# Performance work log

Measured on AMD Instinct MI355X. Metric: run time of the kernel, lower is better.

Reference implementation:

```python
import jax, jax.numpy as jnp
import numpy as np

N_NODES = 50000   # hypergraph nodes
N_EDGES = 20000   # hyperedges
M = 400000        # node-edge incidences (node copies)
L = 800000        # inner GIN graph edges per side
HID = 128
IN_DIM = 128
B = 32            # graphs in batch
C = 10            # num_classes
N_LAYERS = 2
INNER = 2         # inner_num_layers
BN_EPS = 1e-5


def setup_inputs() -> dict:
    key = jax.random.key(0)
    ks = jax.random.split(key, 16)
    s = 0.05
    inp = {}
    inp["x_N"] = jax.random.normal(ks[0], (N_NODES, IN_DIM), jnp.float32)
    # embedding linear
    inp["We"] = jax.random.normal(ks[1], (IN_DIM, HID), jnp.float32) * s
    inp["be"] = jnp.zeros((HID,), jnp.float32)
    # GIN params: [outer_layer, direction(N2E/E2N), inner_conv, mlp_linear, hid, hid]
    inp["Wg"] = jax.random.normal(ks[2], (N_LAYERS, 2, INNER, 2, HID, HID), jnp.float32) * s
    inp["bg"] = jnp.zeros((N_LAYERS, 2, INNER, 2, HID), jnp.float32)
    inp["eps_g"] = jnp.zeros((N_LAYERS, 2, INNER), jnp.float32)
    # eval-mode BatchNorm affine params per inner conv
    inp["gamma"] = jnp.ones((N_LAYERS, 2, INNER, HID), jnp.float32)
    inp["beta"] = jnp.zeros((N_LAYERS, 2, INNER, HID), jnp.float32)
    # per-layer prediction heads
    inp["Wp"] = jax.random.normal(ks[3], (N_LAYERS + 1, HID, C), jnp.float32) * s
    inp["bp"] = jnp.zeros((N_LAYERS + 1, C), jnp.float32)
    # index tensors
    inp["ori_node_idx"] = jax.random.randint(ks[4], (M,), 0, N_NODES)
    inp["node2edge"] = jax.random.randint(ks[5], (M,), 0, N_EDGES)
    inp["edge_index_N"] = jax.random.randint(ks[6], (2, L), 0, M)
    inp["ori_edge_idx"] = jax.random.randint(ks[7], (M,), 0, N_EDGES)
    inp["edge2node"] = jax.random.randint(ks[8], (M,), 0, N_NODES)
    inp["edge_index_E"] = jax.random.randint(ks[9], (2, L), 0, M)
    inp["batch"] = jax.random.randint(ks[10], (M,), 0, B)
    return inp


def _gin(x, src, dst, Wg, bg, eps, gamma, beta):
    # GIN over the copy graph: h = MLP((1+eps)*x + sum_{j->i} x_j), BN (eval), ReLU between convs
    inv_std = 1.0 / jnp.sqrt(1.0 + BN_EPS)
    n = x.shape[0]
    for l in range(INNER):
        agg = jax.ops.segment_sum(x[src], dst, num_segments=n)
        h = (1.0 + eps[l]) * x + agg
        h = jax.nn.relu(h @ Wg[l, 0] + bg[l, 0])
        h = h @ Wg[l, 1] + bg[l, 1]
        h = gamma[l] * h * inv_std + beta[l]
        x = jax.nn.relu(h) if l < INNER - 1 else h
    return x


def reference(x_N, We, be, Wg, bg, eps_g, gamma, beta, Wp, bp,
              ori_node_idx, node2edge, edge_index_N,
              ori_edge_idx, edge2node, edge_index_E, batch):
    node_x = x_N @ We + be                       # [N, HID]
    xs = [node_x]
    for i in range(N_LAYERS):
        # node -> edge: gather copies, inner GIN, segment-sum pool over hyperedges
        nx = node_x[ori_node_idx]                # [M, HID]
        nx = _gin(nx, edge_index_N[0], edge_index_N[1],
                  Wg[i, 0], bg[i, 0], eps_g[i, 0], gamma[i, 0], beta[i, 0])
        edge_x = jax.ops.segment_sum(nx, node2edge, num_segments=N_EDGES)
        edge_x = jax.nn.relu(edge_x)             # EdgeUpdate (dropout off in eval)
        # edge -> node
        ex = edge_x[ori_edge_idx]                # [M, HID]
        ex = _gin(ex, edge_index_E[0], edge_index_E[1],
                  Wg[i, 1], bg[i, 1], eps_g[i, 1], gamma[i, 1], beta[i, 1])
        node_x = jax.ops.segment_sum(ex, edge2node, num_segments=N_NODES)
        node_x = jax.nn.relu(node_x)             # NodeUpdate
        xs.append(node_x)
    score = jnp.zeros((B, C), x_N.dtype)
    for i, x in enumerate(xs):
        pooled = jax.ops.segment_sum(x[ori_node_idx], batch, num_segments=B)
        score = score + pooled @ Wp[i] + bp[i]
    return score
```

## Files before the change

### kernel.cpp

```cpp
#include <hip/hip_runtime.h>
#include <hip/hip_bf16.h>

#define HID 128
static const int N_NODES = 50000;
static const int N_EDGES = 20000;
static const int M_COPIES = 400000;
static const int L_EDGES = 800000;
static const int NBATCH = 32;
static const int NCLS = 10;
#define INV_STD 0.9999950000374997f
#define IDX_CAP 384

typedef __attribute__((ext_vector_type(4))) float f32x4;
typedef __attribute__((ext_vector_type(8))) short short8;
typedef __attribute__((ext_vector_type(8))) unsigned short ushort8;
typedef __attribute__((ext_vector_type(4))) unsigned short u16x4;

__device__ __forceinline__ float bf2f(unsigned short u) {
    union { unsigned u; float f; } v; v.u = ((unsigned)u) << 16; return v.f;
}
__device__ __forceinline__ unsigned short f2bf(float f) {
    union { float f; unsigned u; } v; v.f = f;
    unsigned r = v.u + 0x7FFFu + ((v.u >> 16) & 1u);
    return (unsigned short)(r >> 16);
}
__device__ __forceinline__ void gatomic_add(float* p, float v) {
    unsafeAtomicAdd(p, v);
}

template<int H>
__device__ __forceinline__ void mfma_eighth(const unsigned short* Ws, const short8* xv,
                                            f32x4* acc, int quad, int ln) {
#pragma unroll
    for (int kc = 0; kc < 4; ++kc) {
        short8 wa = *(const short8*)(Ws + (((kc * 4 + quad) * 16) + ln) * 8);
        acc[H] = __builtin_amdgcn_mfma_f32_16x16x32_bf16(wa, xv[kc], acc[H], 0, 0, 0);
    }
}

__global__ __launch_bounds__(256) void prep_w(const float* __restrict__ We,
                                              const float* __restrict__ Wg,
                                              unsigned short* __restrict__ Wt) {
    int t = blockIdx.x * 256 + threadIdx.x;
    if (t >= 17 * 16384) return;
    int mat = t >> 14, rem = t & 16383;
    int n = rem >> 7, k = rem & 127;
    const float* src = (mat == 0) ? We : (Wg + (size_t)(mat - 1) * 16384);
    Wt[t] = f2bf(src[k * 128 + n]);
}

__global__ __launch_bounds__(256) void hist_k(const int* __restrict__ idx, int n,
                                              int* __restrict__ cnt) {
    int t = blockIdx.x * 256 + threadIdx.x;
    if (t < n) atomicAdd(&cnt[idx[t]], 1);
}

__global__ __launch_bounds__(256) void scan1_k(int* __restrict__ a, int n,
                                               int* __restrict__ part) {
    __shared__ int s[256];
    int i = blockIdx.x * 256 + threadIdx.x;
    int v = (i < n) ? a[i] : 0;
    s[threadIdx.x] = v;
    __syncthreads();
#pragma unroll
    for (int d = 1; d < 256; d <<= 1) {
        int t = (threadIdx.x >= d) ? s[threadIdx.x - d] : 0;
        __syncthreads();
        s[threadIdx.x] += t;
        __syncthreads();
    }
    if (i < n) a[i] = s[threadIdx.x] - v;
    if (threadIdx.x == 255) part[blockIdx.x] = s[255];
}

__global__ __launch_bounds__(256) void scan2_k(int* __restrict__ part, int nb) {
    __shared__ int s[256];
    __shared__ int carry;
    if (threadIdx.x == 0) carry = 0;
    __syncthreads();
    for (int base = 0; base < nb; base += 256) {
        int i = base + threadIdx.x;
        int v = (i < nb) ? part[i] : 0;
        s[threadIdx.x] = v;
        __syncthreads();
#pragma unroll
        for (int d = 1; d < 256; d <<= 1) {
            int t = (threadIdx.x >= d) ? s[threadIdx.x - d] : 0;
            __syncthreads();
            s[threadIdx.x] += t;
            __syncthreads();
        }
        if (i < nb) part[i] = carry + s[threadIdx.x] - v;
        __syncthreads();
        if (threadIdx.x == 0) carry += s[255];
        __syncthreads();
    }
}

__global__ __launch_bounds__(256) void scan3_k(int* __restrict__ a, int n,
                                               const int* __restrict__ part) {
    int i = blockIdx.x * 256 + threadIdx.x;
    if (i < n) a[i] += part[blockIdx.x];
}

__global__ __launch_bounds__(256) void fill_edge_k(
    const int* __restrict__ src, const int* __restrict__ dst,
    const int* __restrict__ remap, int n, int* __restrict__ off,
    int* __restrict__ srcs, int* __restrict__ comps) {
    int e = blockIdx.x * 256 + threadIdx.x;
    if (e >= n) return;
    int d = dst[e];
    int pos = atomicAdd(&off[d], 1);
    int s = src[e];
    srcs[pos] = s;
    comps[pos] = remap[s];
}

__global__ __launch_bounds__(256) void fill_pool_k(
    const int* __restrict__ seg, int n, int* __restrict__ off,
    int* __restrict__ items) {
    int m = blockIdx.x * 256 + threadIdx.x;
    if (m >= n) return;
    int pos = atomicAdd(&off[seg[m]], 1);
    items[pos] = m;
}

__global__ __launch_bounds__(256) void segsum_pool(
    const unsigned short* __restrict__ tbl, const int* __restrict__ off,
    const int* __restrict__ items, unsigned short* __restrict__ out, int nseg)
{
    int wave = threadIdx.x >> 6, lane = threadIdx.x & 63;
    int seg = blockIdx.x * 4 + wave;
    if (seg >= nseg) return;
    int start = (seg == 0) ? 0 : off[seg - 1];
    int end = off[seg];
    int g = lane & 15, sub = lane >> 4;
    float a[8] = {0.f, 0.f, 0.f, 0.f, 0.f, 0.f, 0.f, 0.f};
    for (int p = start + sub; p < end; p += 4) {
        int r = items[p];
        ushort8 v = *(const ushort8*)(tbl + (size_t)r * 128 + g * 8);
#pragma unroll
        for (int j = 0; j < 8; ++j) a[j] += bf2f(v[j]);
    }
#pragma unroll
    for (int j = 0; j < 8; ++j) {
        a[j] += __shfl_xor(a[j], 16, 64);
        a[j] += __shfl_xor(a[j], 32, 64);
    }
    if (sub == 0) {
        ushort8 ov;
#pragma unroll
        for (int j = 0; j < 8; ++j) ov[j] = f2bf(fmaxf(a[j], 0.f));
        *(ushort8*)(out + (size_t)seg * 128 + g * 8) = ov;
    }
}

template<bool CONV0>
__global__ __launch_bounds__(256, 7) void fused_conv(
    const unsigned short* __restrict__ tbl,
    const int* __restrict__ self_idx,
    const int* __restrict__ off, const int* __restrict__ items,
    const float* __restrict__ eps_ptr,
    const unsigned short* __restrict__ W1t, const float* __restrict__ b1,
    const unsigned short* __restrict__ W2t, const float* __restrict__ b2,
    const float* __restrict__ gam, const float* __restrict__ bet,
    unsigned short* __restrict__ out)
{
    __shared__ __align__(16) unsigned short Xs[16 * 64 * 8];
    __shared__ __align__(16) unsigned short Ws[16 * 16 * 8];
    __shared__ int sIdx[IDX_CAP];
    __shared__ int meta[192];
    const int tid = threadIdx.x;
    const int row0 = blockIdx.x * 64;

    const int bstart = (row0 == 0) ? 0 : off[row0 - 1];
    const int cnt = off[row0 + 63] - bstart;
    const bool useLds = (cnt <= IDX_CAP);

    if (tid < 64) {
        int gr = row0 + tid;
        meta[tid]       = (gr == 0) ? 0 : off[gr - 1];
        meta[64 + tid]  = off[gr];
        meta[128 + tid] = CONV0 ? self_idx[gr] : gr;
    }
    {
        int n = tid >> 4, gg = tid & 15;
        *(short8*)(Ws + (gg * 16 + n) * 8) = *(const short8*)(W1t + n * 128 + gg * 8);
    }
    if (useLds)
        for (int i = tid; i < cnt; i += 256) sIdx[i] = items[bstart + i];
    __syncthreads();

    const float e = 1.0f + eps_ptr[0];
    const int g = tid & 15;
    const int rb = tid >> 4;
#pragma unroll
    for (int i = 0; i < 4; ++i) {
        int r = rb + 16 * i;
        int start = meta[r], end = meta[64 + r], self = meta[128 + r];
        float a[8];
        ushort8 u = *(const ushort8*)(tbl + (size_t)self * 128 + g * 8);
#pragma unroll
        for (int j = 0; j < 8; ++j) a[j] = e * bf2f(u[j]);
        if (useLds) {
            int pos = start - bstart, pe = end - bstart;
            for (; pos + 2 <= pe; pos += 2) {
                int i0 = sIdx[pos], i1 = sIdx[pos + 1];
                ushort8 v0 = *(const ushort8*)(tbl + (size_t)i0 * 128 + g * 8);
                ushort8 v1 = *(const ushort8*)(tbl + (size_t)i1 * 128 + g * 8);
#pragma unroll
                for (int j = 0; j < 8; ++j) a[j] += bf2f(v0[j]) + bf2f(v1[j]);
            }
            if (pos < pe) {
                int i0 = sIdx[pos];
                ushort8 v0 = *(const ushort8*)(tbl + (size_t)i0 * 128 + g * 8);
#pragma unroll
                for (int j = 0; j < 8; ++j) a[j] += bf2f(v0[j]);
            }
        } else {
            for (int pos = start; pos < end; ++pos) {
                int rr = items[pos];
                ushort8 v = *(const ushort8*)(tbl + (size_t)rr * 128 + g * 8);
#pragma unroll
                for (int j = 0; j < 8; ++j) a[j] += bf2f(v[j]);
            }
        }
        ushort8 xv;
#pragma unroll
        for (int j = 0; j < 8; ++j) xv[j] = f2bf(a[j]);
        *(ushort8*)(Xs + (g * 64 + r) * 8) = xv;
    }
    __syncthreads();

    const int lane = tid & 63;
    const int ln = lane & 15, quad = lane >> 4;
    const int row = (tid >> 6) * 16 + ln;

    short8 xb[4];
#pragma unroll
    for (int kc = 0; kc < 4; ++kc)
        xb[kc] = *(const short8*)(Xs + ((kc * 4 + quad) * 64 + row) * 8);

    f32x4 acc[8];
#pragma unroll
    for (int t = 0; t < 8; ++t) acc[t] = (f32x4){0.f, 0.f, 0.f, 0.f};

    mfma_eighth<0>(Ws, xb, acc, quad, ln);
#pragma unroll
    for (int h = 1; h < 8; ++h) {
        __syncthreads();
        {
            int n = tid >> 4, gg = tid & 15;
            *(short8*)(Ws + (gg * 16 + n) * 8) = *(const short8*)(W1t + (h * 16 + n) * 128 + gg * 8);
        }
        __syncthreads();
        switch (h) {
            case 1: mfma_eighth<1>(Ws, xb, acc, quad, ln); break;
            case 2: mfma_eighth<2>(Ws, xb, acc, quad, ln); break;
            case 3: mfma_eighth<3>(Ws, xb, acc, quad, ln); break;
            case 4: mfma_eighth<4>(Ws, xb, acc, quad, ln); break;
            case 5: mfma_eighth<5>(Ws, xb, acc, quad, ln); break;
            case 6: mfma_eighth<6>(Ws, xb, acc, quad, ln); break;
            default: mfma_eighth<7>(Ws, xb, acc, quad, ln); break;
        }
    }
    {
        const int j0 = (quad & 1) * 4;
#pragma unroll
        for (int t = 0; t < 8; ++t) {
            int p0 = t * 16 + quad * 4;
            f32x4 bv = *(const f32x4*)(b1 + p0);
            u16x4 hp;
#pragma unroll
            for (int i = 0; i < 4; ++i) hp[i] = f2bf(fmaxf(acc[t][i] + bv[i], 0.f));
            *(u16x4*)(Xs + ((p0 >> 3) * 64 + row) * 8 + j0) = hp;
        }
    }
    __syncthreads();
    {
        int n = tid >> 4, gg = tid & 15;
        *(short8*)(Ws + (gg * 16 + n) * 8) = *(const short8*)(W2t + n * 128 + gg * 8);
    }
    __syncthreads();

    short8 hb[4];
#pragma unroll
    for (int kc = 0; kc < 4; ++kc)
        hb[kc] = *(const short8*)(Xs + ((kc * 4 + quad) * 64 + row) * 8);

#pragma unroll
    for (int t = 0; t < 8; ++t) acc[t] = (f32x4){0.f, 0.f, 0.f, 0.f};

    mfma_eighth<0>(Ws, hb, acc, quad, ln);
#pragma unroll
    for (int h = 1; h < 8; ++h) {
        __syncthreads();
        {
            int n = tid >> 4, gg = tid & 15;
            *(short8*)(Ws + (gg * 16 + n) * 8) = *(const short8*)(W2t + (h * 16 + n) * 128 + gg * 8);
        }
        __syncthreads();
        switch (h) {
            case 1: mfma_eighth<1>(Ws, hb, acc, quad, ln); break;
            case 2: mfma_eighth<2>(Ws, hb, acc, quad, ln); break;
            case 3: mfma_eighth<3>(Ws, hb, acc, quad, ln); break;
            case 4: mfma_eighth<4>(Ws, hb, acc, quad, ln); break;
            case 5: mfma_eighth<5>(Ws, hb, acc, quad, ln); break;
            case 6: mfma_eighth<6>(Ws, hb, acc, quad, ln); break;
            default: mfma_eighth<7>(Ws, hb, acc, quad, ln); break;
        }
    }

    const int m = row0 + row;
#pragma unroll
    for (int t = 0; t < 8; ++t) {
        int n0 = t * 16 + quad * 4;
        f32x4 bv = *(const f32x4*)(b2 + n0);
        f32x4 gv = *(const f32x4*)(gam + n0);
        f32x4 tv = *(const f32x4*)(bet + n0);
        u16x4 op;
#pragma unroll
        for (int i = 0; i < 4; ++i) {
            float h = acc[t][i] + bv[i];
            h = gv[i] * h * INV_STD + tv[i];
            if (CONV0) h = fmaxf(h, 0.f);
            op[i] = f2bf(h);
        }
        *(u16x4*)(out + (size_t)m * 128 + n0) = op;
    }
}

__global__ __launch_bounds__(256) void gemm_embed(
    const float* __restrict__ in, const unsigned short* __restrict__ Wt,
    const float* __restrict__ bias, unsigned short* __restrict__ out_bf, int rows)
{
    __shared__ __align__(16) unsigned short Xs[16 * 64 * 8];
    __shared__ __align__(16) unsigned short Ws[16 * 128 * 8];
    int tid = threadIdx.x;
    int row0 = blockIdx.x * 64;
#pragma unroll
    for (int i = 0; i < 8; ++i) {
        int chunk = tid + i * 256;
        int n = chunk >> 4, g = chunk & 15;
        *(short8*)(Ws + (g * 128 + n) * 8) = *(const short8*)(Wt + n * 128 + g * 8);
    }
#pragma unroll
    for (int i = 0; i < 4; ++i) {
        int chunk = tid + i * 256;
        int r = chunk >> 4, g = chunk & 15;
        int gr = row0 + r;
        ushort8 v;
        if (gr < rows) {
            const float* p = in + (size_t)gr * 128 + g * 8;
            f32x4 a0 = *(const f32x4*)p;
            f32x4 a1 = *(const f32x4*)(p + 4);
#pragma unroll
            for (int j = 0; j < 4; ++j) { v[j] = f2bf(a0[j]); v[4 + j] = f2bf(a1[j]); }
        } else {
#pragma unroll
            for (int j = 0; j < 8; ++j) v[j] = 0;
        }
        *(ushort8*)(Xs + (g * 64 + r) * 8) = v;
    }
    __syncthreads();
    int wave = tid >> 6, lane = tid & 63;
    int m0 = wave * 16;
    int ln = lane & 15, quad = lane >> 4;
    f32x4 acc[8];
#pragma unroll
    for (int t = 0; t < 8; ++t) acc[t] = (f32x4){0.f, 0.f, 0.f, 0.f};
#pragma unroll
    for (int kc = 0; kc < 4; ++kc) {
        int g = kc * 4 + quad;
        short8 a = *(const short8*)(Xs + (g * 64 + m0 + ln) * 8);
#pragma unroll
        for (int t = 0; t < 8; ++t) {
            short8 b = *(const short8*)(Ws + (g * 128 + t * 16 + ln) * 8);
            acc[t] = __builtin_amdgcn_mfma_f32_16x16x32_bf16(a, b, acc[t], 0, 0, 0);
        }
    }
#pragma unroll
    for (int t = 0; t < 8; ++t) {
        int col = t * 16 + ln;
        float bi = bias[col];
#pragma unroll
        for (int i = 0; i < 4; ++i) {
            int gr = row0 + m0 + quad * 4 + i;
            if (gr < rows) out_bf[(size_t)gr * 128 + col] = f2bf(acc[t][i] + bi);
        }
    }
}

template<bool ACCUM>
__global__ __launch_bounds__(256) void proj_y(
    const unsigned short* __restrict__ nx, const float* __restrict__ Wp,
    float* __restrict__ y, int rows)
{
    __shared__ float Wl[HID * NCLS];
    for (int i = threadIdx.x; i < HID * NCLS; i += 256) Wl[i] = Wp[i];
    __syncthreads();
    int r = blockIdx.x * 256 + threadIdx.x;
    if (r >= rows) return;
    float acc[NCLS];
#pragma unroll
    for (int c = 0; c < NCLS; ++c) acc[c] = 0.f;
    const unsigned short* xp = nx + (size_t)r * 128;
#pragma unroll 4
    for (int g = 0; g < 16; ++g) {
        ushort8 u = *(const ushort8*)(xp + g * 8);
#pragma unroll
        for (int j = 0; j < 8; ++j) {
            float xv = bf2f(u[j]);
            const float* w = Wl + (g * 8 + j) * NCLS;
#pragma unroll
            for (int c = 0; c < NCLS; ++c) acc[c] += xv * w[c];
        }
    }
    float* yp = y + (size_t)r * NCLS;
#pragma unroll
    for (int c = 0; c < NCLS; ++c) {
        if (ACCUM) yp[c] += acc[c];
        else yp[c] = acc[c];
    }
}

__global__ __launch_bounds__(256) void score_scatter(
    const float* __restrict__ y, const int* __restrict__ ori,
    const int* __restrict__ batch, float* __restrict__ score)
{
    __shared__ float sc[NBATCH * NCLS];
    for (int i = threadIdx.x; i < NBATCH * NCLS; i += 256) sc[i] = 0.f;
    __syncthreads();
    int stride = gridDim.x * 256;
    for (int m = blockIdx.x * 256 + threadIdx.x; m < M_COPIES; m += stride) {
        int r = ori[m], b = batch[m];
        const float* yp = y + (size_t)r * NCLS;
#pragma unroll
        for (int c = 0; c < NCLS; ++c)
            __hip_atomic_fetch_add(&sc[b * NCLS + c], yp[c],
                                   __ATOMIC_RELAXED, __HIP_MEMORY_SCOPE_WORKGROUP);
    }
    __syncthreads();
    for (int i = threadIdx.x; i < NBATCH * NCLS; i += 256) gatomic_add(score + i, sc[i]);
}

__global__ void score_final(const float* __restrict__ score, const float* __restrict__ bp,
                            float* __restrict__ out)
{
    int t = threadIdx.x;
    if (t >= NBATCH * NCLS) return;
    int c = t % NCLS;
    out[t] = score[t] + bp[c] + bp[NCLS + c] + bp[2 * NCLS + c];
}

__global__ void fill_sentinel(float* out, int n, float enc) {
    int t = blockIdx.x * 64 + threadIdx.x;
    if (t < n) out[t] = enc;
}

static inline void build_csr_edge(const int* src, const int* dst, const int* remap,
                                  int nitem, int nseg, int* off, int* part,
                                  int* srcs, int* comps, hipStream_t stream) {
    int nb = (nseg + 255) / 256;
    (void)hipMemsetAsync(off, 0, (size_t)nseg * 4, stream);
    hist_k<<<(nitem + 255) / 256, 256, 0, stream>>>(dst, nitem, off);
    scan1_k<<<nb, 256, 0, stream>>>(off, nseg, part);
    scan2_k<<<1, 256, 0, stream>>>(part, nb);
    scan3_k<<<nb, 256, 0, stream>>>(off, nseg, part);
    fill_edge_k<<<(nitem + 255) / 256, 256, 0, stream>>>(src, dst, remap, nitem, off, srcs, comps);
}
static inline void build_csr_pool(const int* seg, int nitem, int nseg,
                                  int* off, int* part, int* items, hipStream_t stream) {
    int nb = (nseg + 255) / 256;
    (void)hipMemsetAsync(off, 0, (size_t)nseg * 4, stream);
    hist_k<<<(nitem + 255) / 256, 256, 0, stream>>>(seg, nitem, off);
    scan1_k<<<nb, 256, 0, stream>>>(off, nseg, part);
    scan2_k<<<1, 256, 0, stream>>>(part, nb);
    scan3_k<<<nb, 256, 0, stream>>>(off, nseg, part);
    fill_pool_k<<<(nitem + 255) / 256, 256, 0, stream>>>(seg, nitem, off, items);
}

extern "C" void kernel_launch(void* const* d_in, const int* in_sizes, int n_in,
                              void* d_out, int out_size, void* d_ws, size_t ws_size,
                              hipStream_t stream) {
    const float* x_N    = (const float*)d_in[0];
    const float* We     = (const float*)d_in[1];
    const float* be     = (const float*)d_in[2];
    const float* Wg     = (const float*)d_in[3];
    const float* bg     = (const float*)d_in[4];
    const float* eps_g  = (const float*)d_in[5];
    const float* gam    = (const float*)d_in[6];
    const float* bet    = (const float*)d_in[7];
    const float* Wp     = (const float*)d_in[8];
    const float* bp     = (const float*)d_in[9];
    const int* ori_node = (const int*)d_in[10];
    const int* node2edge= (const int*)d_in[11];
    const int* eiN      = (const int*)d_in[12];
    const int* ori_edge = (const int*)d_in[13];
    const int* edge2node= (const int*)d_in[14];
    const int* eiE      = (const int*)d_in[15];
    const int* batch    = (const int*)d_in[16];

    char* p = (char*)d_ws;
    auto take = [&](size_t n) { char* r = p; p += (n + 255) & ~(size_t)255; return r; };
    unsigned short* Wt  = (unsigned short*)take((size_t)17 * 16384 * 2);
    unsigned short* Xb  = (unsigned short*)take((size_t)M_COPIES * 128 * 2);
    unsigned short* Xb2 = (unsigned short*)take((size_t)M_COPIES * 128 * 2);
    unsigned short* nx  = (unsigned short*)take((size_t)N_NODES * 128 * 2);
    unsigned short* ex  = (unsigned short*)take((size_t)N_EDGES * 128 * 2);
    float* y            = (float*)take((size_t)N_NODES * NCLS * 4);
    float* score        = (float*)take((size_t)NBATCH * NCLS * 4);
    int* offN           = (int*)take((size_t)M_COPIES * 4);
    int* offE           = (int*)take((size_t)M_COPIES * 4);
    int* off_n2e        = (int*)take((size_t)N_EDGES * 4);
    int* off_e2n        = (int*)take((size_t)N_NODES * 4);
    int* srcsN          = (int*)take((size_t)L_EDGES * 4);
    int* compsN         = (int*)take((size_t)L_EDGES * 4);
    int* srcsE          = (int*)take((size_t)L_EDGES * 4);
    int* compsE         = (int*)take((size_t)L_EDGES * 4);
    int* it_n2e         = (int*)take((size_t)M_COPIES * 4);
    int* it_e2n         = (int*)take((size_t)M_COPIES * 4);
    int* part           = (int*)take((size_t)2048 * 4);
    size_t need = (size_t)(p - (char*)d_ws);
    if (need > ws_size) {
        fill_sentinel<<<(out_size + 63) / 64, 64, 0, stream>>>(
            (float*)d_out, out_size, 1.0e9f + (float)ws_size);
        return;
    }

    prep_w<<<1088, 256, 0, stream>>>(We, Wg, Wt);
    (void)hipMemsetAsync(score, 0, (size_t)NBATCH * NCLS * 4, stream);

    build_csr_edge(eiN, eiN + L_EDGES, ori_node, L_EDGES, M_COPIES, offN, part, srcsN, compsN, stream);
    build_csr_edge(eiE, eiE + L_EDGES, ori_edge, L_EDGES, M_COPIES, offE, part, srcsE, compsE, stream);
    build_csr_pool(node2edge, M_COPIES, N_EDGES, off_n2e, part, it_n2e, stream);
    build_csr_pool(edge2node, M_COPIES, N_NODES, off_e2n, part, it_e2n, stream);

    gemm_embed<<<(N_NODES + 63) / 64, 256, 0, stream>>>(x_N, Wt, be, nx, N_NODES);
    proj_y<false><<<(N_NODES + 255) / 256, 256, 0, stream>>>(nx, Wp, y, N_NODES);

    const int MBLK = M_COPIES / 64;
    for (int layer = 0; layer < 2; ++layer) {
        for (int dir = 0; dir < 2; ++dir) {
            int cj0 = layer * 4 + dir * 2;
            int cj1 = cj0 + 1;
            const unsigned short* base = (dir == 0) ? nx : ex;
            const int* selfI = (dir == 0) ? ori_node : ori_edge;
            const int* offD  = (dir == 0) ? offN : offE;
            const int* srcsD = (dir == 0) ? srcsN : srcsE;
            const int* compD = (dir == 0) ? compsN : compsE;

            fused_conv<true><<<MBLK, 256, 0, stream>>>(
                base, selfI, offD, compD, eps_g + cj0,
                Wt + (size_t)(1 + cj0 * 2) * 16384, bg + (cj0 * 2) * 128,
                Wt + (size_t)(1 + cj0 * 2 + 1) * 16384, bg + (cj0 * 2 + 1) * 128,
                gam + cj0 * 128, bet + cj0 * 128, Xb);
            fused_conv<false><<<MBLK, 256, 0, stream>>>(
                Xb, nullptr, offD, srcsD, eps_g + cj1,
                Wt + (size_t)(1 + cj1 * 2) * 16384, bg + (cj1 * 2) * 128,
                Wt + (size_t)(1 + cj1 * 2 + 1) * 16384, bg + (cj1 * 2 + 1) * 128,
                gam + cj1 * 128, bet + cj1 * 128, Xb2);
            if (dir == 0) {
                segsum_pool<<<(N_EDGES + 3) / 4, 256, 0, stream>>>(
                    Xb2, off_n2e, it_n2e, ex, N_EDGES);
            } else {
                segsum_pool<<<(N_NODES + 3) / 4, 256, 0, stream>>>(
                    Xb2, off_e2n, it_e2n, nx, N_NODES);
                proj_y<true><<<(N_NODES + 255) / 256, 256, 0, stream>>>(
                    nx, Wp + (layer + 1) * HID * NCLS, y, N_NODES);
            }
        }
    }
    score_scatter<<<256, 256, 0, stream>>>(y, ori_node, batch, score);
    score_final<<<1, 320, 0, stream>>>(score, bp, (float*)d_out);
}
```

Before: 1.529 ms.

## Read GEMM weights directly from global memory and swizzle the activation LDS tile

New measurement: 2.485 ms. 62.6% more time.

```diff
diff --git a/kernel.cpp b/kernel.cpp
--- a/kernel.cpp
+++ b/kernel.cpp
@@ -28,14 +28,9 @@
     unsafeAtomicAdd(p, v);
 }
 
-template<int H>
-__device__ __forceinline__ void mfma_eighth(const unsigned short* Ws, const short8* xv,
-                                            f32x4* acc, int quad, int ln) {
-#pragma unroll
-    for (int kc = 0; kc < 4; ++kc) {
-        short8 wa = *(const short8*)(Ws + (((kc * 4 + quad) * 16) + ln) * 8);
-        acc[H] = __builtin_amdgcn_mfma_f32_16x16x32_bf16(wa, xv[kc], acc[H], 0, 0, 0);
-    }
+__device__ __forceinline__ unsigned short* xs_addr(unsigned short* Xs, int c, int r) {
+    int byte = ((c * 64 + r) * 16) ^ ((c & 7) << 4);
+    return (unsigned short*)((char*)Xs + byte);
 }
 
 __global__ __launch_bounds__(256) void prep_w(const float* __restrict__ We,
@@ -156,7 +151,7 @@
 }
 
 template<bool CONV0>
-__global__ __launch_bounds__(256, 7) void fused_conv(
+__global__ __launch_bounds__(256, 6) void fused_conv(
     const unsigned short* __restrict__ tbl,
     const int* __restrict__ self_idx,
     const int* __restrict__ off, const int* __restrict__ items,
@@ -167,7 +162,6 @@
     unsigned short* __restrict__ out)
 {
     __shared__ __align__(16) unsigned short Xs[16 * 64 * 8];
-    __shared__ __align__(16) unsigned short Ws[16 * 16 * 8];
     __shared__ int sIdx[IDX_CAP];
     __shared__ int meta[192];
     const int tid = threadIdx.x;
@@ -182,10 +176,6 @@
         meta[tid]       = (gr == 0) ? 0 : off[gr - 1];
         meta[64 + tid]  = off[gr];
         meta[128 + tid] = CONV0 ? self_idx[gr] : gr;
-    }
-    {
-        int n = tid >> 4, gg = tid & 15;
-        *(short8*)(Ws + (gg * 16 + n) * 8) = *(const short8*)(W1t + n * 128 + gg * 8);
     }
     if (useLds)
         for (int i = tid; i < cnt; i += 256) sIdx[i] = items[bstart + i];
@@ -228,7 +218,7 @@
         ushort8 xv;
 #pragma unroll
         for (int j = 0; j < 8; ++j) xv[j] = f2bf(a[j]);
-        *(ushort8*)(Xs + (g * 64 + r) * 8) = xv;
+        *(ushort8*)xs_addr(Xs, g, r) = xv;
     }
     __syncthreads();
 
@@ -239,31 +229,24 @@
     short8 xb[4];
 #pragma unroll
     for (int kc = 0; kc < 4; ++kc)
-        xb[kc] = *(const short8*)(Xs + ((kc * 4 + quad) * 64 + row) * 8);
+        xb[kc] = *(const short8*)xs_addr(Xs, kc * 4 + quad, row);
 
     f32x4 acc[8];
 #pragma unroll
     for (int t = 0; t < 8; ++t) acc[t] = (f32x4){0.f, 0.f, 0.f, 0.f};
 
-    mfma_eighth<0>(Ws, xb, acc, quad, ln);
-#pragma unroll
-    for (int h = 1; h < 8; ++h) {
-        __syncthreads();
-        {
-            int n = tid >> 4, gg = tid & 15;
-            *(short8*)(Ws + (gg * 16 + n) * 8) = *(const short8*)(W1t + (h * 16 + n) * 128 + gg * 8);
-        }
-        __syncthreads();
-        switch (h) {
-            case 1: mfma_eighth<1>(Ws, xb, acc, quad, ln); break;
-            case 2: mfma_eighth<2>(Ws, xb, acc, quad, ln); break;
-            case 3: mfma_eighth<3>(Ws, xb, acc, quad, ln); break;
-            case 4: mfma_eighth<4>(Ws, xb, acc, quad, ln); break;
-            case 5: mfma_eighth<5>(Ws, xb, acc, quad, ln); break;
-            case 6: mfma_eighth<6>(Ws, xb, acc, quad, ln); break;
-            default: mfma_eighth<7>(Ws, xb, acc, quad, ln); break;
-        }
-    }
+    {
+        const unsigned short* w1p = W1t + ln * 128 + quad * 8;
+#pragma unroll
+        for (int kc = 0; kc < 4; ++kc) {
+#pragma unroll
+            for (int t = 0; t < 8; ++t) {
+                short8 wa = *(const short8*)(w1p + t * 2048 + kc * 32);
+                acc[t] = __builtin_amdgcn_mfma_f32_16x16x32_bf16(wa, xb[kc], acc[t], 0, 0, 0);
+            }
+        }
+    }
+
     {
         const int j0 = (quad & 1) * 4;
 #pragma unroll
@@ -273,41 +256,27 @@
             u16x4 hp;
 #pragma unroll
             for (int i = 0; i < 4; ++i) hp[i] = f2bf(fmaxf(acc[t][i] + bv[i], 0.f));
-            *(u16x4*)(Xs + ((p0 >> 3) * 64 + row) * 8 + j0) = hp;
-        }
-    }
-    __syncthreads();
+            *(u16x4*)((char*)xs_addr(Xs, p0 >> 3, row) + j0 * 2) = hp;
+        }
+    }
+
+    short8 hb[4];
+#pragma unroll
+    for (int kc = 0; kc < 4; ++kc)
+        hb[kc] = *(const short8*)xs_addr(Xs, kc * 4 + quad, row);
+
+#pragma unroll
+    for (int t = 0; t < 8; ++t) acc[t] = (f32x4){0.f, 0.f, 0.f, 0.f};
+
     {
-        int n = tid >> 4, gg = tid & 15;
-        *(short8*)(Ws + (gg * 16 + n) * 8) = *(const short8*)(W2t + n * 128 + gg * 8);
-    }
-    __syncthreads();
-
-    short8 hb[4];
-#pragma unroll
-    for (int kc = 0; kc < 4; ++kc)
-        hb[kc] = *(const short8*)(Xs + ((kc * 4 + quad) * 64 + row) * 8);
-
-#pragma unroll
-    for (int t = 0; t < 8; ++t) acc[t] = (f32x4){0.f, 0.f, 0.f, 0.f};
-
-    mfma_eighth<0>(Ws, hb, acc, quad, ln);
-#pragma unroll
-    for (int h = 1; h < 8; ++h) {
-        __syncthreads();
-        {
-            int n = tid >> 4, gg = tid & 15;
-            *(short8*)(Ws + (gg * 16 + n) * 8) = *(const short8*)(W2t + (h * 16 + n) * 128 + gg * 8);
-        }
-        __syncthreads();
-        switch (h) {
-            case 1: mfma_eighth<1>(Ws, hb, acc, quad, ln); break;
-            case 2: mfma_eighth<2>(Ws, hb, acc, quad, ln); break;
-            case 3: mfma_eighth<3>(Ws, hb, acc, quad, ln); break;
-            case 4: mfma_eighth<4>(Ws, hb, acc, quad, ln); break;
-            case 5: mfma_eighth<5>(Ws, hb, acc, quad, ln); break;
-            case 6: mfma_eighth<6>(Ws, hb, acc, quad, ln); break;
-            default: mfma_eighth<7>(Ws, hb, acc, quad, ln); break;
+        const unsigned short* w2p = W2t + ln * 128 + quad * 8;
+#pragma unroll
+        for (int kc = 0; kc < 4; ++kc) {
+#pragma unroll
+            for (int t = 0; t < 8; ++t) {
+                short8 wa = *(const short8*)(w2p + t * 2048 + kc * 32);
+                acc[t] = __builtin_amdgcn_mfma_f32_16x16x32_bf16(wa, hb[kc], acc[t], 0, 0, 0);
+            }
         }
     }
 
```
